# Kernel optimization log

Measured on AMD Instinct MI355X. Metric: run time of the kernel, lower is better.

Reference implementation:

```python
import jax, jax.numpy as jnp
import numpy as np

B, S, D = 2, 2048, 1024
H, DQK, DV = 16, 64, 64
DECAY = 0.85


def _fractal_weights(seq_len: int, decay: float) -> np.ndarray:
    # Dragon-curve hierarchical weights: earlier (coarser) positions get higher
    # weight; weight decays by `decay` per hierarchy level. Normalized to sum 1,
    # matching DragonCurveGenerator.get_hierarchical_weights semantics.
    idx = np.arange(seq_len)
    level = np.floor(np.log2(idx + 1)).astype(np.int32)
    w = decay ** level.astype(np.float32)
    return (w / w.sum()).astype(np.float32)


def setup_inputs() -> dict:
    key = jax.random.key(0)
    kx, kq, kk, kv, ko = jax.random.split(key, 5)
    s = 1.0 / np.sqrt(D)
    return {
        "x": jax.random.normal(kx, (B, S, D), dtype=jnp.float32),
        "Wq": jax.random.normal(kq, (D, H * DQK), dtype=jnp.float32) * s,
        "Wk": jax.random.normal(kk, (D, H * DQK), dtype=jnp.float32) * s,
        "Wv": jax.random.normal(kv, (D, H * DV), dtype=jnp.float32) * s,
        "Wo": jax.random.normal(ko, (H * DV, D), dtype=jnp.float32) * s,
        "fractal_weights": jnp.asarray(_fractal_weights(S, DECAY)),
    }


def reference(x, Wq, Wk, Wv, Wo, fractal_weights):
    b, s, _ = x.shape
    # Projections (Linear with bias=False); weights stored as (in, out).
    Q = (x @ Wq).reshape(b, s, H, DQK).transpose(0, 2, 1, 3)  # [B,H,S,Dqk]
    K = (x @ Wk).reshape(b, s, H, DQK).transpose(0, 2, 1, 3)
    V = (x @ Wv).reshape(b, s, H, DV).transpose(0, 2, 1, 3)   # [B,H,S,Dv]
    scale = 1.0 / jnp.sqrt(jnp.asarray(DQK, dtype=x.dtype))
    scores = jnp.einsum("bhqd,bhkd->bhqk", Q, K) * scale      # [B,H,S,S]
    # Multiplicative per-key fractal bias applied BEFORE softmax.
    scores = scores * fractal_weights[None, None, None, :]
    attn = jax.nn.softmax(scores, axis=-1)
    out = jnp.einsum("bhqk,bhkd->bhqd", attn, V)               # [B,H,S,Dv]
    out = out.transpose(0, 2, 1, 3).reshape(b, s, H * DV)
    return out @ Wo                                            # [B,S,D]
```

## Files before the change

### kernel.cpp

```cpp
#include <hip/hip_runtime.h>
#include <hip/hip_bf16.h>
#include <stdint.h>

#define B_  2
#define S_  2048
#define D_  1024
#define H_  16
#define DH_ 64

typedef __attribute__((ext_vector_type(8))) __bf16    bf16x8;
typedef __attribute__((ext_vector_type(8))) _Float16  f16x8;
typedef __attribute__((ext_vector_type(4))) _Float16  f16x4;
typedef __attribute__((ext_vector_type(2))) __fp16    fp16x2;
typedef __attribute__((ext_vector_type(4))) float     f32x4;

__device__ inline unsigned short f2bf(float f) {
    union { float f; uint32_t u; } v; v.f = f;
    uint32_t r = (v.u + 0x7fffu + ((v.u >> 16) & 1u)) >> 16;
    return (unsigned short)r;
}

__device__ __forceinline__ void g2l16(const unsigned short* g, unsigned short* l) {
    __builtin_amdgcn_global_load_lds(
        (const __attribute__((address_space(1))) unsigned int*)g,
        (__attribute__((address_space(3))) unsigned int*)l,
        16, 0, 0);
}


__global__ void convert_x(const float* __restrict__ x, unsigned short* __restrict__ xb, int n) {
    int i = (blockIdx.x * blockDim.x + threadIdx.x) * 4;
    if (i < n) {
        float4 v = *(const float4*)(x + i);
        ushort4 o;
        o.x = f2bf(v.x); o.y = f2bf(v.y); o.z = f2bf(v.z); o.w = f2bf(v.w);
        *(ushort4*)(xb + i) = o;
    }
}

__global__ void transpose_w(const float* __restrict__ s0, const float* __restrict__ s1,
                            const float* __restrict__ s2, const float* __restrict__ s3,
                            unsigned short* __restrict__ d0, unsigned short* __restrict__ d1,
                            unsigned short* __restrict__ d2, unsigned short* __restrict__ d3) {
    __shared__ float tile[32][33];
    const float* src; unsigned short* dst;
    switch (blockIdx.z) {
        case 0: src = s0; dst = d0; break;
        case 1: src = s1; dst = d1; break;
        case 2: src = s2; dst = d2; break;
        default: src = s3; dst = d3; break;
    }
    int n0 = blockIdx.x * 32, k0 = blockIdx.y * 32;
    int tx = threadIdx.x, ty = threadIdx.y;
    for (int j = 0; j < 32; j += 8)
        tile[ty + j][tx] = src[(long)(k0 + ty + j) * 1024 + n0 + tx];
    __syncthreads();
    for (int j = 0; j < 32; j += 8)
        dst[(long)(n0 + ty + j) * 1024 + k0 + tx] = f2bf(tile[tx][ty + j]);
}

__global__ __launch_bounds__(256, 4)
void gemm128(const unsigned short* __restrict__ A, const unsigned short* __restrict__ Bt,
             unsigned short* __restrict__ Qo, unsigned short* __restrict__ Ko,
             unsigned short* __restrict__ Vt,
             const float* __restrict__ fw)
{
    __shared__ __align__(16) unsigned short As[128 * 64];
    __shared__ __align__(16) unsigned short Bs[64 * 64];
    const int tid  = threadIdx.x;
    const int lane = tid & 63, wid = tid >> 6;
    const int quad = lane >> 4, l15 = lane & 15;
    const int bm = blockIdx.y, bn = blockIdx.x;
    const int K = 1024;
    f32x4 acc[2][4] = {};
    const long Abase = (long)bm * 128 * K;
    const long Bbase = (long)bn * 64 * K;

    for (int k0 = 0; k0 < K; k0 += 64) {
        __syncthreads();
#pragma unroll
        for (int i = 0; i < 4; i++) {
            int base = i * 256 + wid * 64;
            int slot = base + lane;
            int row = slot >> 3, cp = slot & 7;
            int c = cp ^ (row & 7);
            g2l16(A + Abase + (long)row * K + k0 + c * 8, &As[base * 8]);
        }
#pragma unroll
        for (int i = 0; i < 2; i++) {
            int base = i * 256 + wid * 64;
            int slot = base + lane;
            int row = slot >> 3, cp = slot & 7;
            int c = cp ^ (row & 7);
            g2l16(Bt + Bbase + (long)row * K + k0 + c * 8, &Bs[base * 8]);
        }
        __syncthreads();
#pragma unroll
        for (int ks = 0; ks < 2; ks++) {
            bf16x8 af[2], bfr[4];
#pragma unroll
            for (int tt = 0; tt < 2; tt++) {
                int ra = wid * 32 + tt * 16 + l15;
                af[tt]  = *(const bf16x8*)(As + ra * 64 + (((ks * 4 + quad) ^ (l15 & 7))) * 8);
            }
#pragma unroll
            for (int tt = 0; tt < 4; tt++) {
                int rb = tt * 16 + l15;
                bfr[tt] = *(const bf16x8*)(Bs + rb * 64 + (((ks * 4 + quad) ^ (l15 & 7))) * 8);
            }
#pragma unroll
            for (int tm = 0; tm < 2; tm++)
#pragma unroll
                for (int tn = 0; tn < 4; tn++)
                    acc[tm][tn] = __builtin_amdgcn_mfma_f32_16x16x32_bf16(af[tm], bfr[tn], acc[tm][tn], 0, 0, 0);
        }
    }

    const float Cq = 0.125f * 1.44269504f;
    for (int tm = 0; tm < 2; tm++)
        for (int tn = 0; tn < 4; tn++)
            for (int r = 0; r < 4; r++) {
                int gm = bm * 128 + wid * 32 + tm * 16 + quad * 4 + r;
                int gn = bn * 64 + tn * 16 + l15;
                float v = acc[tm][tn][r];
                int b = gm >> 11, s = gm & 2047;
                if (gn < 1024) {
                    int h = gn >> 6, d = gn & 63;
                    Qo[(((long)(b * H_ + h) * S_ + s) << 6) + d] = f2bf(v * Cq);
                } else if (gn < 2048) {
                    int g = gn - 1024; int h = g >> 6, d = g & 63;
                    Ko[(((long)(b * H_ + h) * S_ + s) << 6) + d] = f2bf(v * fw[s]);
                } else {
                    int g = gn - 2048; int h = g >> 6, d = g & 63;
                    union { _Float16 h; unsigned short u; } cv;
                    cv.h = (_Float16)v;
                    int sp = s ^ ((d & 8) ? 4 : 0);
                    Vt[((long)(b * H_ + h) * DH_ + d) * S_ + sp] = cv.u;
                }
            }
}

__global__ __launch_bounds__(256, 4)
void gemm_wo(const unsigned short* __restrict__ A, const unsigned short* __restrict__ Bt,
             float* __restrict__ Cout)
{
    __shared__ __align__(16) unsigned short As[64 * 64];
    __shared__ __align__(16) unsigned short Bs[64 * 64];
    const int tid  = threadIdx.x;
    const int lane = tid & 63, wid = tid >> 6;
    const int quad = lane >> 4, l15 = lane & 15;
    const int bm = blockIdx.y, bn = blockIdx.x;
    const int K = 1024;
    f32x4 acc[4] = {};
    const long Abase = (long)bm * 64 * K;
    const long Bbase = (long)bn * 64 * K;

    for (int k0 = 0; k0 < K; k0 += 64) {
        __syncthreads();
#pragma unroll
        for (int i = 0; i < 2; i++) {
            int base = i * 256 + wid * 64;
            int slot = base + lane;
            int row = slot >> 3, cp = slot & 7;
            int c = cp ^ (row & 7);
            g2l16(A + Abase + (long)row * K + k0 + c * 8, &As[base * 8]);
        }
#pragma unroll
        for (int i = 0; i < 2; i++) {
            int base = i * 256 + wid * 64;
            int slot = base + lane;
            int row = slot >> 3, cp = slot & 7;
            int c = cp ^ (row & 7);
            g2l16(Bt + Bbase + (long)row * K + k0 + c * 8, &Bs[base * 8]);
        }
        __syncthreads();
#pragma unroll
        for (int ks = 0; ks < 2; ks++) {
            bf16x8 af, bfr[4];
            {
                int ra = wid * 16 + l15;
                af = *(const bf16x8*)(As + ra * 64 + (((ks * 4 + quad) ^ (l15 & 7))) * 8);
            }
#pragma unroll
            for (int tt = 0; tt < 4; tt++) {
                int rb = tt * 16 + l15;
                bfr[tt] = *(const bf16x8*)(Bs + rb * 64 + (((ks * 4 + quad) ^ (l15 & 7))) * 8);
            }
#pragma unroll
            for (int tn = 0; tn < 4; tn++)
                acc[tn] = __builtin_amdgcn_mfma_f32_16x16x32_bf16(af, bfr[tn], acc[tn], 0, 0, 0);
        }
    }

    for (int tn = 0; tn < 4; tn++)
        for (int r = 0; r < 4; r++) {
            int gm = bm * 64 + wid * 16 + quad * 4 + r;
            int gn = bn * 64 + tn * 16 + l15;
            Cout[(long)gm * 1024 + gn] = acc[tn][r];
        }
}

__global__ __launch_bounds__(512, 4)
void attn_kernel(const unsigned short* __restrict__ Q, const unsigned short* __restrict__ Kb,
                 const unsigned short* __restrict__ Vt,
                 unsigned short* __restrict__ O)
{
    __shared__ __align__(16) unsigned short smem[2][2][2][64 * 64];

    const int tid  = threadIdx.x;
    const int lane = tid & 63, wid = tid >> 6;
    const int half = wid >> 2, sw = wid & 3;
    const int quad = lane >> 4, l15 = lane & 15;
    const int bh = blockIdx.y;
    const int qt = blockIdx.x;

    const unsigned short* Kg = Kb + (long)bh * S_ * DH_;
    const unsigned short* Vg = Vt + (long)bh * (long)DH_ * S_;

    bf16x8 qf[2][2];
#pragma unroll
    for (int st = 0; st < 2; st++) {
        const unsigned short* Qp = Q + ((long)bh * S_ + qt * 128 + sw * 32 + st * 16 + l15) * DH_ + quad * 8;
        qf[st][0] = *(const bf16x8*)(Qp);
        qf[st][1] = *(const bf16x8*)(Qp + 32);
    }

    auto issue = [&](int buf, int kt) {
#pragma unroll
        for (int i = 0; i < 2; i++) {
            int base = i * 256 + sw * 64;
            int slot = base + lane;
            int row = slot >> 3, cp = slot & 7;
            int c = cp ^ (row & 7);
            g2l16(Kg + ((long)(kt * 64 + row) * 64 + c * 8), &smem[half][buf][0][base * 8]);
        }
#pragma unroll
        for (int i = 0; i < 2; i++) {
            int base = i * 256 + sw * 64;
            int slot = base + lane;
            int row = slot >> 3, cp = slot & 7;
            int c = cp ^ (row & 7);
            g2l16(Vg + ((long)row * S_ + kt * 64 + c * 8), &smem[half][buf][1][base * 8]);
        }
    };

    f32x4 oacc[2][4] = {};
    f32x4 lacc[2] = {};
    const f16x8 vone = {(_Float16)1.f, (_Float16)1.f, (_Float16)1.f, (_Float16)1.f,
                        (_Float16)1.f, (_Float16)1.f, (_Float16)1.f, (_Float16)1.f};

    const int kt0 = half * 16;
    issue(0, kt0);
    __syncthreads();

    const int hf = (((quad & 1) ^ ((l15 >> 3) & 1))) * 4;

    for (int t = 0; t < 16; t++) {
        const int cur = t & 1;
        if (t + 1 < 16) issue(1 - cur, kt0 + t + 1);

        const unsigned short* Kc = &smem[half][cur][0][0];
        const unsigned short* Vc = &smem[half][cur][1][0];

        f32x4 sacc[2][4] = {};
#pragma unroll
        for (int kc = 0; kc < 4; kc++) {
            int row = kc * 16 + l15;
            bf16x8 k0 = *(const bf16x8*)(Kc + (row * 8 + (quad       ^ (l15 & 7))) * 8);
            bf16x8 k1 = *(const bf16x8*)(Kc + (row * 8 + ((4 + quad) ^ (l15 & 7))) * 8);
#pragma unroll
            for (int st = 0; st < 2; st++) {
                sacc[st][kc] = __builtin_amdgcn_mfma_f32_16x16x32_bf16(k0, qf[st][0], sacc[st][kc], 0, 0, 0);
                sacc[st][kc] = __builtin_amdgcn_mfma_f32_16x16x32_bf16(k1, qf[st][1], sacc[st][kc], 0, 0, 0);
            }
        }

        f16x8 vfr[2][4];
#pragma unroll
        for (int c = 0; c < 2; c++)
#pragma unroll
            for (int dt = 0; dt < 4; dt++) {
                int row = dt * 16 + l15;
                int p0 = (c * 4 +     (quad >> 1)) ^ (l15 & 7);
                int p1 = (c * 4 + 2 + (quad >> 1)) ^ (l15 & 7);
                f16x4 v0 = *(const f16x4*)(Vc + row * 64 + p0 * 8 + hf);
                f16x4 v1 = *(const f16x4*)(Vc + row * 64 + p1 * 8 + hf);
                vfr[c][dt] = __builtin_shufflevector(v0, v1, 0, 1, 2, 3, 4, 5, 6, 7);
            }

        f16x8 pk8[2][2];
#pragma unroll
        for (int st = 0; st < 2; st++)
#pragma unroll
            for (int c = 0; c < 2; c++) {
                union { uint4 u; f16x8 v; } pku;
#pragma unroll
                for (int hh = 0; hh < 2; hh++) {
                    float p0 = __builtin_amdgcn_exp2f(sacc[st][2 * c + hh][0]);
                    float p1 = __builtin_amdgcn_exp2f(sacc[st][2 * c + hh][1]);
                    float p2 = __builtin_amdgcn_exp2f(sacc[st][2 * c + hh][2]);
                    float p3 = __builtin_amdgcn_exp2f(sacc[st][2 * c + hh][3]);
                    union { fp16x2 h2; unsigned int u; } a, b;
                    a.h2 = __builtin_amdgcn_cvt_pkrtz(p0, p1);
                    b.h2 = __builtin_amdgcn_cvt_pkrtz(p2, p3);
                    if (hh == 0) { pku.u.x = a.u; pku.u.y = b.u; }
                    else         { pku.u.z = a.u; pku.u.w = b.u; }
                }
                pk8[st][c] = pku.v;
            }

#pragma unroll
        for (int c = 0; c < 2; c++) {
            lacc[0] = __builtin_amdgcn_mfma_f32_16x16x32_f16(pk8[0][c], vone, lacc[0], 0, 0, 0);
            lacc[1] = __builtin_amdgcn_mfma_f32_16x16x32_f16(pk8[1][c], vone, lacc[1], 0, 0, 0);
#pragma unroll
            for (int dt = 0; dt < 4; dt++) {
                oacc[0][dt] = __builtin_amdgcn_mfma_f32_16x16x32_f16(pk8[0][c], vfr[c][dt], oacc[0][dt], 0, 0, 0);
                oacc[1][dt] = __builtin_amdgcn_mfma_f32_16x16x32_f16(pk8[1][c], vfr[c][dt], oacc[1][dt], 0, 0, 0);
            }
        }

        __syncthreads();
    }

    float* ov = (float*)&smem[0][0][0][0];
    float* lv = ov + 128 * 66;

    if (half == 1) {
#pragma unroll
        for (int st = 0; st < 2; st++) {
#pragma unroll
            for (int dt = 0; dt < 4; dt++)
#pragma unroll
                for (int r = 0; r < 4; r++) {
                    int qr = sw * 32 + st * 16 + quad * 4 + r;
                    ov[qr * 66 + dt * 16 + l15] = oacc[st][dt][r];
                }
            if (l15 == 0) {
#pragma unroll
                for (int r = 0; r < 4; r++)
                    lv[sw * 32 + st * 16 + quad * 4 + r] = lacc[st][r];
            }
        }
    }
    __syncthreads();

    if (half == 0) {
        int b = bh >> 4, h = bh & 15;
#pragma unroll
        for (int st = 0; st < 2; st++)
#pragma unroll
            for (int r = 0; r < 4; r++) {
                int qr = sw * 32 + st * 16 + quad * 4 + r;
                float inv = 1.0f / (lacc[st][r] + lv[qr]);
                int srow = qt * 128 + qr;
#pragma unroll
                for (int dt = 0; dt < 4; dt++) {
                    float val = oacc[st][dt][r] + ov[qr * 66 + dt * 16 + l15];
                    O[((long)(b * S_ + srow)) * 1024 + h * DH_ + dt * 16 + l15] = f2bf(val * inv);
                }
            }
    }
}


extern "C" void kernel_launch(void* const* d_in, const int* in_sizes, int n_in,
                              void* d_out, int out_size, void* d_ws, size_t ws_size,
                              hipStream_t stream)
{
    const float* x  = (const float*)d_in[0];
    const float* Wq = (const float*)d_in[1];
    const float* Wk = (const float*)d_in[2];
    const float* Wv = (const float*)d_in[3];
    const float* Wo = (const float*)d_in[4];
    const float* fw = (const float*)d_in[5];
    float* out = (float*)d_out;

    char* ws = (char*)d_ws;
    unsigned short* xb    = (unsigned short*)(ws);
    unsigned short* WqkvT = (unsigned short*)(ws + 8388608);
    unsigned short* WoT   = (unsigned short*)(ws + 14680064);
    unsigned short* Qb    = (unsigned short*)(ws + 16777216);
    unsigned short* Kb    = (unsigned short*)(ws + 25165824);
    unsigned short* Vt    = (unsigned short*)(ws + 33554432);
    unsigned short* Ob    = xb;

    convert_x<<<dim3((B_ * S_ * D_) / 4 / 256), dim3(256), 0, stream>>>(x, xb, B_ * S_ * D_);
    transpose_w<<<dim3(32, 32, 4), dim3(32, 8), 0, stream>>>(
        Wq, Wk, Wv, Wo,
        WqkvT, WqkvT + 1024 * 1024, WqkvT + 2 * 1024 * 1024, WoT);
    gemm128<<<dim3(48, 32), dim3(256), 0, stream>>>(xb, WqkvT, Qb, Kb, Vt, fw);
    attn_kernel<<<dim3(S_ / 128, B_ * H_), dim3(512), 0, stream>>>(Qb, Kb, Vt, Ob);
    gemm_wo<<<dim3(16, 64), dim3(256), 0, stream>>>(Ob, WoT, out);
}
```

Measured before the change: 190.0 us.

## Enlarge QKV GEMM tile to 128x128 and attention query tile to 256 rows

The QKV projection GEMM goes from a 128x64 to a 128x128 block tile with a 2x2 warp layout, so each wave computes a 64x64 sub-tile and reuses more operand data per LDS load. The attention kernel now gives each block 256 query rows (64 per wave) instead of 128, so each K/V tile loaded into shared memory serves twice as many queries. The cross-half epilogue reduction is split into two passes to fit the existing shared buffer. The costs are more registers per thread, which forces lower occupancy (launch bounds 2), and half as many blocks, which could leave compute units idle on the grid (256 attention blocks).

```diff
diff --git a/kernel.cpp b/kernel.cpp
--- a/kernel.cpp
+++ b/kernel.cpp
@@ -59,57 +59,53 @@
         dst[(long)(n0 + ty + j) * 1024 + k0 + tx] = f2bf(tile[tx][ty + j]);
 }
 
-__global__ __launch_bounds__(256, 4)
+__global__ __launch_bounds__(256, 2)
 void gemm128(const unsigned short* __restrict__ A, const unsigned short* __restrict__ Bt,
              unsigned short* __restrict__ Qo, unsigned short* __restrict__ Ko,
              unsigned short* __restrict__ Vt,
              const float* __restrict__ fw)
 {
     __shared__ __align__(16) unsigned short As[128 * 64];
-    __shared__ __align__(16) unsigned short Bs[64 * 64];
+    __shared__ __align__(16) unsigned short Bs[128 * 64];
     const int tid  = threadIdx.x;
     const int lane = tid & 63, wid = tid >> 6;
     const int quad = lane >> 4, l15 = lane & 15;
+    const int wm = wid >> 1, wn = wid & 1;
     const int bm = blockIdx.y, bn = blockIdx.x;
     const int K = 1024;
-    f32x4 acc[2][4] = {};
+    f32x4 acc[4][4] = {};
     const long Abase = (long)bm * 128 * K;
-    const long Bbase = (long)bn * 64 * K;
+    const long Bbase = (long)bn * 128 * K;
 
     for (int k0 = 0; k0 < K; k0 += 64) {
         __syncthreads();
 #pragma unroll
         for (int i = 0; i < 4; i++) {
-            int base = i * 256 + wid * 64;
-            int slot = base + lane;
-            int row = slot >> 3, cp = slot & 7;
-            int c = cp ^ (row & 7);
-            g2l16(A + Abase + (long)row * K + k0 + c * 8, &As[base * 8]);
-        }
-#pragma unroll
-        for (int i = 0; i < 2; i++) {
-            int base = i * 256 + wid * 64;
-            int slot = base + lane;
-            int row = slot >> 3, cp = slot & 7;
-            int c = cp ^ (row & 7);
-            g2l16(Bt + Bbase + (long)row * K + k0 + c * 8, &Bs[base * 8]);
+            int slot = i * 256 + wid * 64 + lane;
+            int row = slot >> 3, cp = slot & 7;
+            int c = cp ^ (row & 7);
+            g2l16(A + Abase + (long)row * K + k0 + c * 8, &As[(i * 256 + wid * 64) * 8]);
+        }
+#pragma unroll
+        for (int i = 0; i < 4; i++) {
+            int slot = i * 256 + wid * 64 + lane;
+            int row = slot >> 3, cp = slot & 7;
+            int c = cp ^ (row & 7);
+            g2l16(Bt + Bbase + (long)row * K + k0 + c * 8, &Bs[(i * 256 + wid * 64) * 8]);
         }
         __syncthreads();
 #pragma unroll
         for (int ks = 0; ks < 2; ks++) {
-            bf16x8 af[2], bfr[4];
-#pragma unroll
-            for (int tt = 0; tt < 2; tt++) {
-                int ra = wid * 32 + tt * 16 + l15;
-                af[tt]  = *(const bf16x8*)(As + ra * 64 + (((ks * 4 + quad) ^ (l15 & 7))) * 8);
-            }
-#pragma unroll
-            for (int tt = 0; tt < 4; tt++) {
-                int rb = tt * 16 + l15;
-                bfr[tt] = *(const bf16x8*)(Bs + rb * 64 + (((ks * 4 + quad) ^ (l15 & 7))) * 8);
-            }
-#pragma unroll
-            for (int tm = 0; tm < 2; tm++)
+            bf16x8 af[4], bfr[4];
+#pragma unroll
+            for (int t = 0; t < 4; t++) {
+                int ra = wm * 64 + t * 16 + l15;
+                af[t]  = *(const bf16x8*)(As + ra * 64 + (((ks * 4 + quad) ^ (l15 & 7))) * 8);
+                int rb = wn * 64 + t * 16 + l15;
+                bfr[t] = *(const bf16x8*)(Bs + rb * 64 + (((ks * 4 + quad) ^ (l15 & 7))) * 8);
+            }
+#pragma unroll
+            for (int tm = 0; tm < 4; tm++)
 #pragma unroll
                 for (int tn = 0; tn < 4; tn++)
                     acc[tm][tn] = __builtin_amdgcn_mfma_f32_16x16x32_bf16(af[tm], bfr[tn], acc[tm][tn], 0, 0, 0);
@@ -117,11 +113,11 @@
     }
 
     const float Cq = 0.125f * 1.44269504f;
-    for (int tm = 0; tm < 2; tm++)
+    for (int tm = 0; tm < 4; tm++)
         for (int tn = 0; tn < 4; tn++)
             for (int r = 0; r < 4; r++) {
-                int gm = bm * 128 + wid * 32 + tm * 16 + quad * 4 + r;
-                int gn = bn * 64 + tn * 16 + l15;
+                int gm = bm * 128 + wm * 64 + tm * 16 + quad * 4 + r;
+                int gn = bn * 128 + wn * 64 + tn * 16 + l15;
                 float v = acc[tm][tn][r];
                 int b = gm >> 11, s = gm & 2047;
                 if (gn < 1024) {
@@ -200,7 +196,7 @@
         }
 }
 
-__global__ __launch_bounds__(512, 4)
+__global__ __launch_bounds__(512, 2)
 void attn_kernel(const unsigned short* __restrict__ Q, const unsigned short* __restrict__ Kb,
                  const unsigned short* __restrict__ Vt,
                  unsigned short* __restrict__ O)
@@ -217,10 +213,10 @@
     const unsigned short* Kg = Kb + (long)bh * S_ * DH_;
     const unsigned short* Vg = Vt + (long)bh * (long)DH_ * S_;
 
-    bf16x8 qf[2][2];
-#pragma unroll
-    for (int st = 0; st < 2; st++) {
-        const unsigned short* Qp = Q + ((long)bh * S_ + qt * 128 + sw * 32 + st * 16 + l15) * DH_ + quad * 8;
+    bf16x8 qf[4][2];
+#pragma unroll
+    for (int st = 0; st < 4; st++) {
+        const unsigned short* Qp = Q + ((long)bh * S_ + qt * 256 + sw * 64 + st * 16 + l15) * DH_ + quad * 8;
         qf[st][0] = *(const bf16x8*)(Qp);
         qf[st][1] = *(const bf16x8*)(Qp + 32);
     }
@@ -244,8 +240,8 @@
         }
     };
 
-    f32x4 oacc[2][4] = {};
-    f32x4 lacc[2] = {};
+    f32x4 oacc[4][4] = {};
+    f32x4 lacc[4] = {};
     const f16x8 vone = {(_Float16)1.f, (_Float16)1.f, (_Float16)1.f, (_Float16)1.f,
                         (_Float16)1.f, (_Float16)1.f, (_Float16)1.f, (_Float16)1.f};
 
@@ -262,14 +258,14 @@
         const unsigned short* Kc = &smem[half][cur][0][0];
         const unsigned short* Vc = &smem[half][cur][1][0];
 
-        f32x4 sacc[2][4] = {};
+        f32x4 sacc[4][4] = {};
 #pragma unroll
         for (int kc = 0; kc < 4; kc++) {
             int row = kc * 16 + l15;
             bf16x8 k0 = *(const bf16x8*)(Kc + (row * 8 + (quad       ^ (l15 & 7))) * 8);
             bf16x8 k1 = *(const bf16x8*)(Kc + (row * 8 + ((4 + quad) ^ (l15 & 7))) * 8);
 #pragma unroll
-            for (int st = 0; st < 2; st++) {
+            for (int st = 0; st < 4; st++) {
                 sacc[st][kc] = __builtin_amdgcn_mfma_f32_16x16x32_bf16(k0, qf[st][0], sacc[st][kc], 0, 0, 0);
                 sacc[st][kc] = __builtin_amdgcn_mfma_f32_16x16x32_bf16(k1, qf[st][1], sacc[st][kc], 0, 0, 0);
             }
@@ -288,9 +284,9 @@
                 vfr[c][dt] = __builtin_shufflevector(v0, v1, 0, 1, 2, 3, 4, 5, 6, 7);
             }
 
-        f16x8 pk8[2][2];
-#pragma unroll
-        for (int st = 0; st < 2; st++)
+        f16x8 pk8[4][2];
+#pragma unroll
+        for (int st = 0; st < 4; st++)
 #pragma unroll
             for (int c = 0; c < 2; c++) {
                 union { uint4 u; f16x8 v; } pku;
@@ -311,13 +307,14 @@
 
 #pragma unroll
         for (int c = 0; c < 2; c++) {
-            lacc[0] = __builtin_amdgcn_mfma_f32_16x16x32_f16(pk8[0][c], vone, lacc[0], 0, 0, 0);
-            lacc[1] = __builtin_amdgcn_mfma_f32_16x16x32_f16(pk8[1][c], vone, lacc[1], 0, 0, 0);
-#pragma unroll
-            for (int dt = 0; dt < 4; dt++) {
-                oacc[0][dt] = __builtin_amdgcn_mfma_f32_16x16x32_f16(pk8[0][c], vfr[c][dt], oacc[0][dt], 0, 0, 0);
-                oacc[1][dt] = __builtin_amdgcn_mfma_f32_16x16x32_f16(pk8[1][c], vfr[c][dt], oacc[1][dt], 0, 0, 0);
-            }
+#pragma unroll
+            for (int st = 0; st < 4; st++)
+                lacc[st] = __builtin_amdgcn_mfma_f32_16x16x32_f16(pk8[st][c], vone, lacc[st], 0, 0, 0);
+#pragma unroll
+            for (int dt = 0; dt < 4; dt++)
+#pragma unroll
+                for (int st = 0; st < 4; st++)
+                    oacc[st][dt] = __builtin_amdgcn_mfma_f32_16x16x32_f16(pk8[st][c], vfr[c][dt], oacc[st][dt], 0, 0, 0);
         }
 
         __syncthreads();
@@ -325,41 +322,47 @@
 
     float* ov = (float*)&smem[0][0][0][0];
     float* lv = ov + 128 * 66;
-
-    if (half == 1) {
-#pragma unroll
-        for (int st = 0; st < 2; st++) {
-#pragma unroll
-            for (int dt = 0; dt < 4; dt++)
+    int b = bh >> 4, h = bh & 15;
+
+#pragma unroll
+    for (int p = 0; p < 2; p++) {
+        if (half == 1) {
+#pragma unroll
+            for (int si = 0; si < 2; si++) {
+                int st = 2 * p + si;
+#pragma unroll
+                for (int dt = 0; dt < 4; dt++)
+#pragma unroll
+                    for (int r = 0; r < 4; r++) {
+                        int qr = sw * 32 + si * 16 + quad * 4 + r;
+                        ov[qr * 66 + dt * 16 + l15] = oacc[st][dt][r];
+                    }
+                if (l15 == 0) {
+#pragma unroll
+                    for (int r = 0; r < 4; r++)
+                        lv[sw * 32 + si * 16 + quad * 4 + r] = lacc[st][r];
+                }
+            }
+        }
+        __syncthreads();
+        if (half == 0) {
+#pragma unroll
+            for (int si = 0; si < 2; si++) {
+                int st = 2 * p + si;
 #pragma unroll
                 for (int r = 0; r < 4; r++) {
-                    int qr = sw * 32 + st * 16 + quad * 4 + r;
-                    ov[qr * 66 + dt * 16 + l15] = oacc[st][dt][r];
+                    int qr = sw * 32 + si * 16 + quad * 4 + r;
+                    float inv = 1.0f / (lacc[st][r] + lv[qr]);
+                    int srow = qt * 256 + sw * 64 + st * 16 + quad * 4 + r;
+#pragma unroll
+                    for (int dt = 0; dt < 4; dt++) {
+                        float val = oacc[st][dt][r] + ov[qr * 66 + dt * 16 + l15];
+                        O[((long)(b * S_ + srow)) * 1024 + h * DH_ + dt * 16 + l15] = f2bf(val * inv);
+                    }
                 }
-            if (l15 == 0) {
-#pragma unroll
-                for (int r = 0; r < 4; r++)
-                    lv[sw * 32 + st * 16 + quad * 4 + r] = lacc[st][r];
-            }
-        }
-    }
-    __syncthreads();
-
-    if (half == 0) {
-        int b = bh >> 4, h = bh & 15;
-#pragma unroll
-        for (int st = 0; st < 2; st++)
-#pragma unroll
-            for (int r = 0; r < 4; r++) {
-                int qr = sw * 32 + st * 16 + quad * 4 + r;
-                float inv = 1.0f / (lacc[st][r] + lv[qr]);
-                int srow = qt * 128 + qr;
-#pragma unroll
-                for (int dt = 0; dt < 4; dt++) {
-                    float val = oacc[st][dt][r] + ov[qr * 66 + dt * 16 + l15];
-                    O[((long)(b * S_ + srow)) * 1024 + h * DH_ + dt * 16 + l15] = f2bf(val * inv);
-                }
-            }
+            }
+        }
+        __syncthreads();
     }
 }
 
@@ -389,7 +392,7 @@
     transpose_w<<<dim3(32, 32, 4), dim3(32, 8), 0, stream>>>(
         Wq, Wk, Wv, Wo,
         WqkvT, WqkvT + 1024 * 1024, WqkvT + 2 * 1024 * 1024, WoT);
-    gemm128<<<dim3(48, 32), dim3(256), 0, stream>>>(xb, WqkvT, Qb, Kb, Vt, fw);
-    attn_kernel<<<dim3(S_ / 128, B_ * H_), dim3(512), 0, stream>>>(Qb, Kb, Vt, Ob);
+    gemm128<<<dim3(24, 32), dim3(256), 0, stream>>>(xb, WqkvT, Qb, Kb, Vt, fw);
+    attn_kernel<<<dim3(S_ / 256, B_ * H_), dim3(512), 0, stream>>>(Qb, Kb, Vt, Ob);
     gemm_wo<<<dim3(16, 64), dim3(256), 0, stream>>>(Ob, WoT, out);
 }
```

After: 180.1 us. 1.06x faster.
